# Kernel optimization log

Measured on AMD Instinct MI355X. Metric: run time of the kernel, lower is better.

Reference implementation:

```python
import jax, jax.numpy as jnp
import numpy as np

N_NODES = 50000   # r_mat is [N_NODES, N_NODES] sparse
N_REL = 1000      # number of relations (rows of dual_layer)
D = 128           # node / relation feature dim
NNZ = 800000      # number of edges (nnz of r_mat)


def setup_inputs() -> dict:
    key = jax.random.key(0)
    k1, k2, k3, k4, k5, k6 = jax.random.split(key, 6)
    return {
        "inlayer": jax.random.normal(k1, (N_NODES, D), jnp.float32),
        "dual_layer": jax.random.normal(k2, (N_REL, D), jnp.float32),
        # Conv1d(in=D, out=1, kernel=1): weight [1, D, 1] -> vector [D], bias [1]
        "conv_w": jax.random.normal(k3, (D,), jnp.float32) * (1.0 / np.sqrt(D)),
        "conv_b": jax.random.normal(k4, (1,), jnp.float32) * 0.01,
        # COO indices of r_mat: row = destination node, col = source node
        "edge_idx": jax.random.randint(k5, (2, NNZ), 0, N_NODES, dtype=jnp.int32),
        # r_mat._values(): integer relation id per edge
        "edge_rel": jax.random.randint(k6, (NNZ,), 0, N_REL, dtype=jnp.int32),
    }


def reference(inlayer, dual_layer, conv_w, conv_b, edge_idx, edge_rel):
    # conv1d with kernel_size=1 over [1, D, n_rel] == per-relation linear -> [n_rel]
    scores = dual_layer @ conv_w + conv_b[0]
    # gather per-edge logit by relation id
    logits = scores[edge_rel]                                  # [nnz]
    # NOTE: original applies leaky_relu then softmax GLOBALLY over all nnz edges
    coefs = jax.nn.softmax(jax.nn.leaky_relu(logits))          # [nnz]
    row, col = edge_idx[0], edge_idx[1]
    # sparse-dense matmul: out[r] = sum_{e: row[e]=r} coefs[e] * inlayer[col[e]]
    out = jax.ops.segment_sum(coefs[:, None] * inlayer[col], row,
                              num_segments=N_NODES)            # [N, D]
    # act_func=None path of the original forward
    return out
```

## Files before the change

### kernel.cpp

```cpp
#include <hip/hip_runtime.h>
#include <hip/hip_fp16.h>
#include <math.h>

#define N_NODES 50000
#define N_REL   1000
#define D       128
#define NNZ     800000

#define RB    512
#define NBIN  98
#define CAP   10240
#define CH    2048
#define NCH   ((NNZ + CH - 1) / CH)
#define K1T   512
#define K1E   (CH / K1T)
#define SRB   64
#define CAPL  1536

__global__ void __launch_bounds__(K1T)
k1_kernel(const int* __restrict__ rows, const int* __restrict__ cols,
          const int* __restrict__ rel, const float* __restrict__ dual,
          const float* __restrict__ conv_w, const float* __restrict__ conv_b,
          const float* __restrict__ inlayer, float* __restrict__ exp_scores,
          unsigned* __restrict__ relcnt, unsigned* __restrict__ bincur,
          unsigned long long* __restrict__ binbuf, __half2* __restrict__ hinl) {
    __shared__ unsigned long long sbuf[CH];
    __shared__ unsigned char sbin[CH];
    __shared__ unsigned lcnt[NBIN], lstart[NBIN], lgb[NBIN];
    __shared__ unsigned lrel[N_REL];
    __shared__ unsigned w0sum;
    int t = threadIdx.x;
    int gtid = blockIdx.x * K1T + t;
    int lane = t & 63;

    int wid = gtid >> 6;
    if (wid < N_REL) {
        const float* row = dual + (long)wid * D;
        float s = row[lane] * conv_w[lane] + row[lane + 64] * conv_w[lane + 64];
        #pragma unroll
        for (int off = 32; off > 0; off >>= 1) s += __shfl_down(s, off);
        if (lane == 0) {
            float v = s + conv_b[0];
            v = (v >= 0.f) ? v : 0.01f * v;
            exp_scores[wid] = expf(v);
        }
    }

    const float4* src4 = (const float4*)inlayer;
    uint2* dst2 = (uint2*)hinl;
    for (int i = gtid; i < N_NODES * D / 4; i += NCH * K1T) {
        float4 f = src4[i];
        __half2 h0 = __floats2half2_rn(f.x, f.y);
        __half2 h1 = __floats2half2_rn(f.z, f.w);
        uint2 o; o.x = *(unsigned*)&h0; o.y = *(unsigned*)&h1;
        dst2[i] = o;
    }

    if (t < NBIN) lcnt[t] = 0;
    for (int i = t; i < N_REL; i += K1T) lrel[i] = 0;
    __syncthreads();

    int n = NNZ - blockIdx.x * CH; if (n > CH) n = CH;
    int base4 = blockIdx.x * (CH / 4);

    int       ebin[K1E];
    unsigned  erank[K1E];
    unsigned long long epack[K1E];
    bool has = (4 * t < n);
    int4 rr, cc, qq;
    if (has) {
        rr = ((const int4*)rows)[base4 + t];
        cc = ((const int4*)cols)[base4 + t];
        qq = ((const int4*)rel)[base4 + t];
    }
    #pragma unroll
    for (int k = 0; k < K1E; ++k) {
        if (has) {
            int r = (k == 0) ? rr.x : (k == 1) ? rr.y : (k == 2) ? rr.z : rr.w;
            int c = (k == 0) ? cc.x : (k == 1) ? cc.y : (k == 2) ? cc.z : cc.w;
            int q = (k == 0) ? qq.x : (k == 1) ? qq.y : (k == 2) ? qq.z : qq.w;
            int b = r >> 9;
            epack[k] = (unsigned long long)(unsigned)c
                     | ((unsigned long long)(unsigned)q << 16)
                     | ((unsigned long long)(unsigned)(r & 511) << 26);
            ebin[k] = b;
            erank[k] = atomicAdd(&lcnt[b], 1u);
            atomicAdd(&lrel[q], 1u);
        } else ebin[k] = -1;
    }
    __syncthreads();

    unsigned v = (t < NBIN) ? lcnt[t] : 0u;
    if (t < 128) {
        #pragma unroll
        for (int off = 1; off < 64; off <<= 1) {
            unsigned y = __shfl_up(v, off);
            if (lane >= off) v += y;
        }
        if (t == 63) w0sum = v;
    }
    __syncthreads();
    if (t >= 64 && t < 128) v += w0sum;
    if (t < NBIN) {
        lstart[t] = v - lcnt[t];
        lgb[t] = atomicAdd(&bincur[t * 16], lcnt[t]);
    }
    for (int i = t; i < N_REL; i += K1T) {
        unsigned cv = lrel[i];
        if (cv) atomicAdd(&relcnt[i], cv);
    }
    __syncthreads();

    #pragma unroll
    for (int k = 0; k < K1E; ++k) {
        if (ebin[k] >= 0) {
            unsigned p = lstart[ebin[k]] + erank[k];
            sbuf[p] = epack[k];
            sbin[p] = (unsigned char)ebin[k];
        }
    }
    __syncthreads();

    #pragma unroll
    for (int k = 0; k < K1E; ++k) {
        int j = k * K1T + t;
        if (j < n) {
            int b = sbin[j];
            unsigned slot = lgb[b] + (unsigned)j - lstart[b];
            if (slot < CAP)
                binbuf[(unsigned long long)b * CAP + slot] = sbuf[j];
        }
    }
}

__global__ void __launch_bounds__(512)
k2_kernel(const unsigned* __restrict__ bincur,
          const unsigned long long* __restrict__ binbuf,
          const float* __restrict__ exp_scores,
          const unsigned* __restrict__ relcnt,
          const __half2* __restrict__ hinl, float* __restrict__ out) {
    __shared__ unsigned list[CAPL];
    __shared__ unsigned cnt[SRB], ex[SRB], cur[SRB];
    int t = threadIdx.x, lane = t & 63, w = t >> 6;
    int b   = blockIdx.x >> 3;
    int sub = blockIdx.x & 7;

    if (t < SRB) cnt[t] = 0;

    float dsum = 0.f;
    for (int i = lane; i < N_REL; i += 64)
        dsum += (float)relcnt[i] * exp_scores[i];
    #pragma unroll
    for (int off = 32; off > 0; off >>= 1) dsum += __shfl_down(dsum, off);
    float inv = 1.0f / __shfl(dsum, 0);

    __syncthreads();

    unsigned nb = bincur[b * 16]; if (nb > CAP) nb = CAP;
    const unsigned long long* bb = binbuf + (unsigned long long)b * CAP;

    for (unsigned e = t; e < nb; e += 512u) {
        unsigned u = (unsigned)(bb[e] >> 26) & 511u;
        if ((u >> 6) == (unsigned)sub) atomicAdd(&cnt[u & 63u], 1u);
    }
    __syncthreads();

    if (t < 64) {
        unsigned c0 = cnt[t];
        unsigned v = c0;
        #pragma unroll
        for (int off = 1; off < 64; off <<= 1) {
            unsigned y = __shfl_up(v, off);
            if (lane >= off) v += y;
        }
        ex[t] = v - c0;
        cur[t] = v - c0;
    }
    __syncthreads();

    for (unsigned e = t; e < nb; e += 512u) {
        unsigned long long pk = bb[e];
        unsigned u = (unsigned)(pk >> 26) & 511u;
        if ((u >> 6) == (unsigned)sub) {
            unsigned idx = atomicAdd(&cur[u & 63u], 1u);
            if (idx < CAPL) list[idx] = (unsigned)pk & 0x3FFFFFFu;
        }
    }
    __syncthreads();

    int quad = lane >> 4;
    int l16  = lane & 15;
    for (int i = 0; i < 8; ++i) {
        int rl = w * 8 + i;
        int node = b * RB + sub * SRB + rl;
        int s0 = (int)ex[rl];
        int e0 = s0 + (int)cnt[rl];
        if (e0 > CAPL) e0 = CAPL;
        float a0=0.f,a1=0.f,a2=0.f,a3=0.f,a4=0.f,a5=0.f,a6=0.f,a7=0.f;
        for (int base = s0; base < e0; base += 64) {
            int rem = e0 - base; if (rem > 64) rem = 64;
            int px = 0, py = 0;
            if (lane < rem) {
                unsigned pk = list[base + lane];
                px = (int)(pk & 0xFFFFu);
                py = __float_as_int(exp_scores[pk >> 16]);
            }
            for (int j = 0; j < rem; j += 16) {
                #pragma unroll
                for (int k = 0; k < 16; k += 4) {
                    if (j + k < rem) {
                        int idx = j + k + quad;
                        int   c = __shfl(px, idx);
                        float wv = __int_as_float(__shfl(py, idx));
                        const __half2* hp = hinl + (long)c * (D / 2) + l16 * 4;
                        uint4 hv = *(const uint4*)hp;
                        float2 f0 = __half22float2(*(const __half2*)&hv.x);
                        float2 f1 = __half22float2(*(const __half2*)&hv.y);
                        float2 f2 = __half22float2(*(const __half2*)&hv.z);
                        float2 f3 = __half22float2(*(const __half2*)&hv.w);
                        a0 += wv * f0.x; a1 += wv * f0.y;
                        a2 += wv * f1.x; a3 += wv * f1.y;
                        a4 += wv * f2.x; a5 += wv * f2.y;
                        a6 += wv * f3.x; a7 += wv * f3.y;
                    }
                }
            }
        }
        #define COMB(x) x += __shfl(x, lane ^ 16); x += __shfl(x, lane ^ 32);
        COMB(a0) COMB(a1) COMB(a2) COMB(a3) COMB(a4) COMB(a5) COMB(a6) COMB(a7)
        #undef COMB
        if (lane < 32 && node < N_NODES) {
            float4 v;
            int hi = (lane >> 4) & 1;
            if (hi) { v.x = a4*inv; v.y = a5*inv; v.z = a6*inv; v.w = a7*inv; }
            else    { v.x = a0*inv; v.y = a1*inv; v.z = a2*inv; v.w = a3*inv; }
            *(float4*)(out + (long)node * D + l16 * 8 + hi * 4) = v;
        }
    }
}

extern "C" void kernel_launch(void* const* d_in, const int* in_sizes, int n_in,
                              void* d_out, int out_size, void* d_ws, size_t ws_size,
                              hipStream_t stream) {
    const float* inlayer  = (const float*)d_in[0];
    const float* dual     = (const float*)d_in[1];
    const float* conv_w   = (const float*)d_in[2];
    const float* conv_b   = (const float*)d_in[3];
    const int*   edge_idx = (const int*)d_in[4];
    const int*   edge_rel = (const int*)d_in[5];
    float* out = (float*)d_out;
    const int* rows = edge_idx;
    const int* cols = edge_idx + NNZ;

    char* ws = (char*)d_ws;
    float*              exp_scores = (float*)             (ws);
    unsigned*           relcnt     = (unsigned*)          (ws + 4096);
    unsigned*           bincur     = (unsigned*)          (ws + 8192);
    unsigned long long* binbuf     = (unsigned long long*)(ws + 16384);
    __half2*            hinl       = (__half2*)           (ws + 16384 + 8028160);

    hipMemsetAsync(ws + 4096, 0, 12288, stream);

    k1_kernel<<<NCH, K1T, 0, stream>>>(rows, cols, edge_rel, dual, conv_w, conv_b,
                                       inlayer, exp_scores, relcnt, bincur,
                                       binbuf, hinl);
    k2_kernel<<<NBIN * 8, 512, 0, stream>>>(bincur, binbuf, exp_scores, relcnt,
                                            hinl, out);
}
```

Baseline: 147.5 us.

## Stage filtered bin entries in LDS and remap blocks to spread bins across XCDs

k2 now reads each bin's packed entries from global memory only once: the first pass filters the entries for its sub-range into an LDS list while counting. The scatter pass then reads that LDS list instead of re-reading the global bin buffer. Block indices are also remapped so the eight consecutive blocks sharing a hardware slot handle different bins. The grid is padded to 104*8 blocks, and the extra blocks exit early. This costs an extra 6KB of LDS per block and a global atomic-like shared counter.

```diff
diff --git a/kernel.cpp b/kernel.cpp
--- a/kernel.cpp
+++ b/kernel.cpp
@@ -139,13 +139,19 @@
           const float* __restrict__ exp_scores,
           const unsigned* __restrict__ relcnt,
           const __half2* __restrict__ hinl, float* __restrict__ out) {
+    __shared__ unsigned ulist[CAPL];
     __shared__ unsigned list[CAPL];
     __shared__ unsigned cnt[SRB], ex[SRB], cur[SRB];
+    __shared__ unsigned total;
     int t = threadIdx.x, lane = t & 63, w = t >> 6;
-    int b   = blockIdx.x >> 3;
-    int sub = blockIdx.x & 7;
+    int x = blockIdx.x & 7;
+    int j = blockIdx.x >> 3;
+    int b = x + 8 * (j >> 3);
+    int sub = j & 7;
+    if (b >= NBIN) return;
 
     if (t < SRB) cnt[t] = 0;
+    if (t == 0) total = 0;
 
     float dsum = 0.f;
     for (int i = lane; i < N_REL; i += 64)
@@ -160,8 +166,14 @@
     const unsigned long long* bb = binbuf + (unsigned long long)b * CAP;
 
     for (unsigned e = t; e < nb; e += 512u) {
-        unsigned u = (unsigned)(bb[e] >> 26) & 511u;
-        if ((u >> 6) == (unsigned)sub) atomicAdd(&cnt[u & 63u], 1u);
+        unsigned long long pk = bb[e];
+        unsigned u = (unsigned)(pk >> 26) & 511u;
+        if ((u >> 6) == (unsigned)sub) {
+            unsigned lo = (unsigned)pk;
+            unsigned idx = atomicAdd(&total, 1u);
+            if (idx < CAPL) ulist[idx] = lo;
+            atomicAdd(&cnt[lo >> 26], 1u);
+        }
     }
     __syncthreads();
 
@@ -178,13 +190,11 @@
     }
     __syncthreads();
 
-    for (unsigned e = t; e < nb; e += 512u) {
-        unsigned long long pk = bb[e];
-        unsigned u = (unsigned)(pk >> 26) & 511u;
-        if ((u >> 6) == (unsigned)sub) {
-            unsigned idx = atomicAdd(&cur[u & 63u], 1u);
-            if (idx < CAPL) list[idx] = (unsigned)pk & 0x3FFFFFFu;
-        }
+    unsigned tot = total; if (tot > CAPL) tot = CAPL;
+    for (unsigned i = t; i < tot; i += 512u) {
+        unsigned lo = ulist[i];
+        unsigned idx = atomicAdd(&cur[lo >> 26], 1u);
+        if (idx < CAPL) list[idx] = lo & 0x3FFFFFFu;
     }
     __syncthreads();
 
@@ -205,11 +215,11 @@
                 px = (int)(pk & 0xFFFFu);
                 py = __float_as_int(exp_scores[pk >> 16]);
             }
-            for (int j = 0; j < rem; j += 16) {
+            for (int jj = 0; jj < rem; jj += 16) {
                 #pragma unroll
                 for (int k = 0; k < 16; k += 4) {
-                    if (j + k < rem) {
-                        int idx = j + k + quad;
+                    if (jj + k < rem) {
+                        int idx = jj + k + quad;
                         int   c = __shfl(px, idx);
                         float wv = __int_as_float(__shfl(py, idx));
                         const __half2* hp = hinl + (long)c * (D / 2) + l16 * 4;
@@ -264,6 +274,6 @@
     k1_kernel<<<NCH, K1T, 0, stream>>>(rows, cols, edge_rel, dual, conv_w, conv_b,
                                        inlayer, exp_scores, relcnt, bincur,
                                        binbuf, hinl);
-    k2_kernel<<<NBIN * 8, 512, 0, stream>>>(bincur, binbuf, exp_scores, relcnt,
-                                            hinl, out);
+    k2_kernel<<<104 * 8, 512, 0, stream>>>(bincur, binbuf, exp_scores, relcnt,
+                                           hinl, out);
 }
```

After: 140.6 us. -4.7%, faster.
